# Kernel optimization log

Measured on AMD Instinct MI355X. Metric: run time of the kernel, lower is better.

The kernel has to match this reference:

```python
import jax, jax.numpy as jnp
import numpy as np

B, S, D_MODEL = 2, 2048, 1024
NUM_HEADS = 16
D_HEAD = D_MODEL // NUM_HEADS
THETA = 10000.0


def setup_inputs() -> dict:
    key = jax.random.key(0)
    ks = jax.random.split(key, 5)
    std = float(np.sqrt(2.0 / (D_MODEL + D_MODEL)))
    return {
        "x": jax.random.normal(ks[0], (B, S, D_MODEL), dtype=jnp.float32),
        "wq": jax.random.normal(ks[1], (D_MODEL, D_MODEL), dtype=jnp.float32) * std,
        "wk": jax.random.normal(ks[2], (D_MODEL, D_MODEL), dtype=jnp.float32) * std,
        "wv": jax.random.normal(ks[3], (D_MODEL, D_MODEL), dtype=jnp.float32) * std,
        "wo": jax.random.normal(ks[4], (D_MODEL, D_MODEL), dtype=jnp.float32) * std,
    }


def _apply_rope(x):
    # x: [b, h, s, d]; interleaved even/odd RoPE rotation
    d = x.shape[-1]
    s = x.shape[-2]
    inv_freq = 1.0 / (THETA ** (jnp.arange(0, d, 2, dtype=x.dtype) / d))  # [d/2]
    pos = jnp.arange(s, dtype=x.dtype)
    freqs = pos[:, None] * inv_freq[None, :]  # [s, d/2]
    cos, sin = jnp.cos(freqs), jnp.sin(freqs)
    x_even = x[..., 0::2]
    x_odd = x[..., 1::2]
    rot_even = x_even * cos - x_odd * sin
    rot_odd = x_even * sin + x_odd * cos
    # interleave back: stack pairs on a new trailing axis then flatten
    return jnp.stack([rot_even, rot_odd], axis=-1).reshape(x.shape)


def reference(x, wq, wk, wv, wo):
    b, s, _ = x.shape
    # Linear applies weight [d_out, d_in] as x @ W^T
    q = jnp.einsum('bsd,ed->bse', x, wq)
    k = jnp.einsum('bsd,ed->bse', x, wk)
    v = jnp.einsum('bsd,ed->bse', x, wv)
    # [b, s, h*dh] -> [b, h, s, dh]
    q = q.reshape(b, s, NUM_HEADS, D_HEAD).transpose(0, 2, 1, 3)
    k = k.reshape(b, s, NUM_HEADS, D_HEAD).transpose(0, 2, 1, 3)
    v = v.reshape(b, s, NUM_HEADS, D_HEAD).transpose(0, 2, 1, 3)
    q = _apply_rope(q)
    k = _apply_rope(k)
    scores = jnp.einsum('bhqd,bhkd->bhqk', q, k) / jnp.sqrt(jnp.asarray(D_HEAD, x.dtype))
    causal = jnp.tril(jnp.ones((s, s), dtype=bool))  # allowed positions
    scores = jnp.where(causal, scores, -jnp.inf)
    attn = jax.nn.softmax(scores, axis=-1)
    out = jnp.einsum('bhqk,bhkd->bhqd', attn, v)
    out = out.transpose(0, 2, 1, 3).reshape(b, s, NUM_HEADS * D_HEAD)
    return jnp.einsum('bsd,ed->bse', out, wo)
```

## Files before the change

### kernel.cpp

```cpp
#include <hip/hip_runtime.h>
#include <stdint.h>

typedef unsigned short u16;
typedef __attribute__((ext_vector_type(8))) short bf16x8;
typedef __attribute__((ext_vector_type(4))) short bf16x4;
typedef __attribute__((ext_vector_type(4))) float f32x4;
typedef __attribute__((ext_vector_type(4))) unsigned short u16x4;
typedef __attribute__((ext_vector_type(2))) unsigned u32x2;

#define S_ 2048
#define E_ 1024
#define QSCALE 0.18033688011112042f

__device__ __forceinline__ u16 f2bf(float f) {
  union { float f; unsigned u; } v; v.f = f;
  unsigned u = v.u;
  unsigned r = (u + 0x7FFFu + ((u >> 16) & 1u)) >> 16;
  return (u16)r;
}
__device__ __forceinline__ float bf2f(u16 h) {
  union { unsigned u; float f; } v; v.u = ((unsigned)h) << 16;
  return v.f;
}
__device__ __forceinline__ unsigned cvtpk(float a, float b) {
  unsigned r;
  asm("v_cvt_pk_bf16_f32 %0, %1, %2" : "=v"(r) : "v"(a), "v"(b));
  return r;
}
__device__ __forceinline__ bf16x4 pk4(float a, float b, float c, float d) {
  union { u32x2 u; bf16x4 v; } U;
  U.u[0] = cvtpk(a, b);
  U.u[1] = cvtpk(c, d);
  return U.v;
}

typedef __attribute__((address_space(3))) void lds_void;
__device__ __forceinline__ unsigned lds_off(void* p) {
  return (unsigned)(unsigned long long)(lds_void*)p;
}
__device__ __forceinline__ void glds16(const u16* g, u16* l) {
  __builtin_amdgcn_global_load_lds(
      (const __attribute__((address_space(1))) void*)g,
      (__attribute__((address_space(3))) void*)l, 16, 0, 0);
}

__global__ void k_cast5(const float* __restrict__ x,
                        const float* __restrict__ wq, const float* __restrict__ wk,
                        const float* __restrict__ wv, const float* __restrict__ wo,
                        u16* __restrict__ xb, u16* __restrict__ wqb, u16* __restrict__ wkb,
                        u16* __restrict__ wvb, u16* __restrict__ wob) {
  int i = blockIdx.x * blockDim.x + threadIdx.x;
  const float* src; u16* dst; int off;
  if (i < 1048576) { src = x; dst = xb; off = i; }
  else {
    int j = i - 1048576;
    int w = j >> 18; off = j & 262143;
    src = (w == 0) ? wq : (w == 1) ? wk : (w == 2) ? wv : wo;
    dst = (w == 0) ? wqb : (w == 1) ? wkb : (w == 2) ? wvb : wob;
  }
  float4 v = *((const float4*)src + off);
  u16x4 o;
  o.x = f2bf(v.x); o.y = f2bf(v.y); o.z = f2bf(v.z); o.w = f2bf(v.w);
  *((u16x4*)dst + off) = o;
}

__global__ __launch_bounds__(256) void k_gemm(
    const u16* __restrict__ A,
    const u16* __restrict__ W0, const u16* __restrict__ W1, const u16* __restrict__ W2,
    void* O0, void* O1, void* O2, int outF32)
{
  __shared__ __align__(16) u16 As[2][128 * 32];
  __shared__ __align__(16) u16 Ws[2][128 * 32];
  int tid = threadIdx.x;
  int wid = tid >> 6, lane = tid & 63;
  int lg = lane >> 4, lr = lane & 15;
  int wsel = blockIdx.y >> 3, nb = blockIdx.y & 7;
  const u16* W = (wsel == 0) ? W0 : ((wsel == 1) ? W1 : W2);
  void* O = (wsel == 0) ? O0 : ((wsel == 1) ? O1 : O2);
  int m0 = blockIdx.x * 128;
  int n0 = nb * 128;
  int wr = wid >> 1, wc = wid & 1;

  f32x4 acc[4][4];
#pragma unroll
  for (int m = 0; m < 4; m++)
#pragma unroll
    for (int n = 0; n < 4; n++) acc[m][n] = (f32x4){0.f, 0.f, 0.f, 0.f};

  int srow = tid >> 2;
  int schunk = (tid & 3) ^ ((tid >> 3) & 3);
  const u16* ag = A + (size_t)(m0 + srow) * 1024 + schunk * 8;
  const u16* wg = W + (size_t)(n0 + srow) * 1024 + schunk * 8;

  int buf = 0;
  glds16(ag, &As[0][tid * 8]);
  glds16(ag + 65536, &As[0][tid * 8 + 2048]);
  glds16(wg, &Ws[0][tid * 8]);
  glds16(wg + 65536, &Ws[0][tid * 8 + 2048]);
  __syncthreads();

  for (int kt = 0; kt < 1024; kt += 32) {
    if (kt + 32 < 1024) {
      glds16(ag + kt + 32, &As[buf ^ 1][tid * 8]);
      glds16(ag + kt + 32 + 65536, &As[buf ^ 1][tid * 8 + 2048]);
      glds16(wg + kt + 32, &Ws[buf ^ 1][tid * 8]);
      glds16(wg + kt + 32 + 65536, &Ws[buf ^ 1][tid * 8 + 2048]);
    }
    bf16x8 af[4], wf[4];
#pragma unroll
    for (int m = 0; m < 4; m++) {
      int row = wr * 64 + m * 16 + lr;
      af[m] = *(const bf16x8*)&As[buf][row * 32 + ((lg ^ ((row >> 1) & 3)) * 8)];
    }
#pragma unroll
    for (int n = 0; n < 4; n++) {
      int row = wc * 64 + n * 16 + lr;
      wf[n] = *(const bf16x8*)&Ws[buf][row * 32 + ((lg ^ ((row >> 1) & 3)) * 8)];
    }
    __builtin_amdgcn_s_setprio(1);
#pragma unroll
    for (int m = 0; m < 4; m++)
#pragma unroll
      for (int n = 0; n < 4; n++)
        acc[m][n] = __builtin_amdgcn_mfma_f32_16x16x32_bf16(af[m], wf[n], acc[m][n], 0, 0, 0);
    __builtin_amdgcn_s_setprio(0);
    __syncthreads();
    buf ^= 1;
  }

#pragma unroll
  for (int m = 0; m < 4; m++) {
    int gr = m0 + wr * 64 + m * 16 + lg * 4;
#pragma unroll
    for (int n = 0; n < 4; n++) {
      int gc = n0 + wc * 64 + n * 16 + lr;
#pragma unroll
      for (int r = 0; r < 4; r++) {
        if (outF32) ((float*)O)[(size_t)(gr + r) * 1024 + gc] = acc[m][n][r];
        else ((u16*)O)[(size_t)(gr + r) * 1024 + gc] = f2bf(acc[m][n][r]);
      }
    }
  }
}

__global__ void k_rope(u16* __restrict__ Q, u16* __restrict__ K) {
  int idx = blockIdx.x * blockDim.x + threadIdx.x;
  int p = idx & 511;
  int srow = idx >> 9;
  int s = srow & (S_ - 1);
  int i = p & 31;
  float ang = (float)s * exp2f(-0.415241012f * (float)i);
  float sn, c;
  __sincosf(ang, &sn, &c);
  unsigned* qp = (unsigned*)Q + idx;
  unsigned qv = *qp;
  float e = bf2f((u16)(qv & 0xffff)), o = bf2f((u16)(qv >> 16));
  float re = (e * c - o * sn) * QSCALE, ro = (e * sn + o * c) * QSCALE;
  *qp = cvtpk(re, ro);
  unsigned* kp = (unsigned*)K + idx;
  unsigned kv = *kp;
  e = bf2f((u16)(kv & 0xffff)); o = bf2f((u16)(kv >> 16));
  re = e * c - o * sn; ro = e * sn + o * c;
  *kp = cvtpk(re, ro);
}

__global__ __launch_bounds__(256) void k_attn(
    const u16* __restrict__ Q, const u16* __restrict__ K,
    const u16* __restrict__ V, u16* __restrict__ AO)
{
  __shared__ __align__(16) u16 Ks[64 * 64];
  __shared__ __align__(16) u16 Vs[64 * 64];
  int tid = threadIdx.x;
  int wid = tid >> 6, lane = tid & 63;
  int lg = lane >> 4, lr = lane & 15;
  int bh = blockIdx.x;
  int qb = 15 - (int)blockIdx.y;
  int q0 = qb * 128 + wid * 32;
  size_t base = (size_t)(bh >> 4) * (2048u * 1024u) + (size_t)(bh & 15) * 64;

  const u16* qrow = Q + base + (size_t)(q0 + lr) * 1024 + lg * 8;
  bf16x8 qf0a = *(const bf16x8*)(qrow);
  bf16x8 qf1a = *(const bf16x8*)(qrow + 32);
  bf16x8 qf0b = *(const bf16x8*)(qrow + 16 * 1024);
  bf16x8 qf1b = *(const bf16x8*)(qrow + 16 * 1024 + 32);

  int srow = tid >> 3;
  int sch = tid & 7;
  const u16* kg = K + base + (size_t)srow * 1024 + sch * 8;
  const u16* vg = V + base + (size_t)srow * 1024 + sch * 8;
  int kwb0 = ((srow)*128 + sch * 16) ^ ((srow & 7) << 4);
  int kwb1 = ((srow + 32) * 128 + sch * 16) ^ ((srow & 7) << 4);
  int vwi0 = (srow >> 4) * 1024 + (sch >> 1) * 256 + (srow & 15) * 16 + (sch & 1) * 8;
  int vwi1 = ((srow + 32) >> 4) * 1024 + (sch >> 1) * 256 + (srow & 15) * 16 + (sch & 1) * 8;

  bf16x8 kr0 = *(const bf16x8*)(kg);
  bf16x8 kr1 = *(const bf16x8*)(kg + 32 * 1024);
  bf16x8 vr0 = *(const bf16x8*)(vg);
  bf16x8 vr1 = *(const bf16x8*)(vg + 32 * 1024);
  const u16* kgp = kg + 64 * 1024;
  const u16* vgp = vg + 64 * 1024;

  float ma = -1e30f, mb = -1e30f, lsa = 0.f, lsb = 0.f;
  f32x4 oa[4], ob[4];
#pragma unroll
  for (int c = 0; c < 4; c++) {
    oa[c] = (f32x4){0.f, 0.f, 0.f, 0.f};
    ob[c] = (f32x4){0.f, 0.f, 0.f, 0.f};
  }

  int qga = q0 + lr;
  int qgb = q0 + 16 + lr;
  int ntw = (q0 >> 6) + 1;
  int ntb = 2 * qb + 2;
  unsigned vrd = lds_off(Vs) + (unsigned)(lane * 8);

  for (int t = 0; t < ntb; ++t) {
    __syncthreads();
    *(bf16x8*)((char*)Ks + kwb0) = kr0;
    *(bf16x8*)((char*)Ks + kwb1) = kr1;
    *(bf16x8*)(&Vs[vwi0]) = vr0;
    *(bf16x8*)(&Vs[vwi1]) = vr1;
    __syncthreads();
    if (t + 1 < ntb) {
      kr0 = *(const bf16x8*)(kgp);
      kr1 = *(const bf16x8*)(kgp + 32 * 1024);
      vr0 = *(const bf16x8*)(vgp);
      vr1 = *(const bf16x8*)(vgp + 32 * 1024);
      kgp += 64 * 1024;
      vgp += 64 * 1024;
    }
    if (t >= ntw) continue;

    f32x4 sa[4], sb[4];
    int kv0 = t * 64;
    __builtin_amdgcn_s_setprio(1);
#pragma unroll
    for (int sub = 0; sub < 4; ++sub) {
      int row = sub * 16 + lr;
      int swz = (row & 7) << 4;
      bf16x8 kf0 = *(const bf16x8*)((const char*)Ks + ((row * 128 + lg * 16) ^ swz));
      bf16x8 kf1 = *(const bf16x8*)((const char*)Ks + ((row * 128 + 64 + lg * 16) ^ swz));
      f32x4 z = (f32x4){0.f, 0.f, 0.f, 0.f};
      z = __builtin_amdgcn_mfma_f32_16x16x32_bf16(kf0, qf0a, z, 0, 0, 0);
      sa[sub] = __builtin_amdgcn_mfma_f32_16x16x32_bf16(kf1, qf1a, z, 0, 0, 0);
      f32x4 z2 = (f32x4){0.f, 0.f, 0.f, 0.f};
      z2 = __builtin_amdgcn_mfma_f32_16x16x32_bf16(kf0, qf0b, z2, 0, 0, 0);
      sb[sub] = __builtin_amdgcn_mfma_f32_16x16x32_bf16(kf1, qf1b, z2, 0, 0, 0);
    }
    __builtin_amdgcn_s_setprio(0);
    if (t == ntw - 1) {
#pragma unroll
      for (int sub = 0; sub < 4; ++sub)
#pragma unroll
        for (int j = 0; j < 4; ++j) {
          int kvg = kv0 + sub * 16 + lg * 4 + j;
          sa[sub][j] = (kvg <= qga) ? sa[sub][j] : -1e30f;
          sb[sub][j] = (kvg <= qgb) ? sb[sub][j] : -1e30f;
        }
    }
    float tma = fmaxf(fmaxf(fmaxf(sa[0][0], sa[0][1]), fmaxf(sa[0][2], sa[0][3])),
                      fmaxf(fmaxf(sa[1][0], sa[1][1]), fmaxf(sa[1][2], sa[1][3])));
    tma = fmaxf(tma, fmaxf(fmaxf(fmaxf(sa[2][0], sa[2][1]), fmaxf(sa[2][2], sa[2][3])),
                           fmaxf(fmaxf(sa[3][0], sa[3][1]), fmaxf(sa[3][2], sa[3][3]))));
    float tmb = fmaxf(fmaxf(fmaxf(sb[0][0], sb[0][1]), fmaxf(sb[0][2], sb[0][3])),
                      fmaxf(fmaxf(sb[1][0], sb[1][1]), fmaxf(sb[1][2], sb[1][3])));
    tmb = fmaxf(tmb, fmaxf(fmaxf(fmaxf(sb[2][0], sb[2][1]), fmaxf(sb[2][2], sb[2][3])),
                           fmaxf(fmaxf(sb[3][0], sb[3][1]), fmaxf(sb[3][2], sb[3][3]))));
    tma = fmaxf(tma, __shfl_xor(tma, 16));
    tma = fmaxf(tma, __shfl_xor(tma, 32));
    tmb = fmaxf(tmb, __shfl_xor(tmb, 16));
    tmb = fmaxf(tmb, __shfl_xor(tmb, 32));
    if (!__all((tma <= ma + 8.f) && (tmb <= mb + 8.f))) {
      float mna = fmaxf(ma, tma), mnb = fmaxf(mb, tmb);
      float ca = __builtin_amdgcn_exp2f(ma - mna);
      float cb = __builtin_amdgcn_exp2f(mb - mnb);
      ma = mna; mb = mnb;
      lsa *= ca; lsb *= cb;
#pragma unroll
      for (int c = 0; c < 4; ++c) {
        oa[c][0] *= ca; oa[c][1] *= ca; oa[c][2] *= ca; oa[c][3] *= ca;
        ob[c][0] *= cb; ob[c][1] *= cb; ob[c][2] *= cb; ob[c][3] *= cb;
      }
    }
    bf16x4 pa[4], pb[4];
#pragma unroll
    for (int sub = 0; sub < 4; ++sub) {
      float a0 = __builtin_amdgcn_exp2f(sa[sub][0] - ma);
      float a1 = __builtin_amdgcn_exp2f(sa[sub][1] - ma);
      float a2 = __builtin_amdgcn_exp2f(sa[sub][2] - ma);
      float a3 = __builtin_amdgcn_exp2f(sa[sub][3] - ma);
      lsa += (a0 + a1) + (a2 + a3);
      pa[sub] = pk4(a0, a1, a2, a3);
      float b0 = __builtin_amdgcn_exp2f(sb[sub][0] - mb);
      float b1 = __builtin_amdgcn_exp2f(sb[sub][1] - mb);
      float b2 = __builtin_amdgcn_exp2f(sb[sub][2] - mb);
      float b3 = __builtin_amdgcn_exp2f(sb[sub][3] - mb);
      lsb += (b0 + b1) + (b2 + b3);
      pb[sub] = pk4(b0, b1, b2, b3);
    }
#pragma unroll
    for (int sub = 0; sub < 4; ++sub) {
      unsigned wa = vrd + (unsigned)(sub * 2048);
      bf16x4 va0, va1, va2, va3;
      asm volatile("ds_read_b64_tr_b16 %0, %1" : "=v"(va0) : "v"(wa));
      asm volatile("ds_read_b64_tr_b16 %0, %1 offset:512" : "=v"(va1) : "v"(wa));
      asm volatile("ds_read_b64_tr_b16 %0, %1 offset:1024" : "=v"(va2) : "v"(wa));
      asm volatile("ds_read_b64_tr_b16 %0, %1 offset:1536" : "=v"(va3) : "v"(wa));
      asm volatile("s_waitcnt lgkmcnt(0)" ::: "memory");
      __builtin_amdgcn_sched_barrier(0);
      __builtin_amdgcn_s_setprio(1);
      oa[0] = __builtin_amdgcn_mfma_f32_16x16x16bf16_1k(va0, pa[sub], oa[0], 0, 0, 0);
      oa[1] = __builtin_amdgcn_mfma_f32_16x16x16bf16_1k(va1, pa[sub], oa[1], 0, 0, 0);
      oa[2] = __builtin_amdgcn_mfma_f32_16x16x16bf16_1k(va2, pa[sub], oa[2], 0, 0, 0);
      oa[3] = __builtin_amdgcn_mfma_f32_16x16x16bf16_1k(va3, pa[sub], oa[3], 0, 0, 0);
      ob[0] = __builtin_amdgcn_mfma_f32_16x16x16bf16_1k(va0, pb[sub], ob[0], 0, 0, 0);
      ob[1] = __builtin_amdgcn_mfma_f32_16x16x16bf16_1k(va1, pb[sub], ob[1], 0, 0, 0);
      ob[2] = __builtin_amdgcn_mfma_f32_16x16x16bf16_1k(va2, pb[sub], ob[2], 0, 0, 0);
      ob[3] = __builtin_amdgcn_mfma_f32_16x16x16bf16_1k(va3, pb[sub], ob[3], 0, 0, 0);
      __builtin_amdgcn_s_setprio(0);
    }
  }

  float lta = lsa + __shfl_xor(lsa, 16);
  lta += __shfl_xor(lta, 32);
  float ltb = lsb + __shfl_xor(lsb, 16);
  ltb += __shfl_xor(ltb, 32);
  float inva = 1.0f / lta;
  float invb = 1.0f / ltb;
  u16* orowa = AO + base + (size_t)(q0 + lr) * 1024;
  u16* orowb = orowa + 16 * 1024;
#pragma unroll
  for (int c = 0; c < 4; c++) {
    u32x2 pka, pkb;
    pka[0] = cvtpk(oa[c][0] * inva, oa[c][1] * inva);
    pka[1] = cvtpk(oa[c][2] * inva, oa[c][3] * inva);
    *(u32x2*)&orowa[c * 16 + lg * 4] = pka;
    pkb[0] = cvtpk(ob[c][0] * invb, ob[c][1] * invb);
    pkb[1] = cvtpk(ob[c][2] * invb, ob[c][3] * invb);
    *(u32x2*)&orowb[c * 16 + lg * 4] = pkb;
  }
}

extern "C" void kernel_launch(void* const* d_in, const int* in_sizes, int n_in,
                              void* d_out, int out_size, void* d_ws, size_t ws_size,
                              hipStream_t stream) {
  const float* x = (const float*)d_in[0];
  const float* wq = (const float*)d_in[1];
  const float* wk = (const float*)d_in[2];
  const float* wv = (const float*)d_in[3];
  const float* wo = (const float*)d_in[4];

  char* ws = (char*)d_ws;
  u16* xb  = (u16*)(ws);
  u16* wqb = (u16*)(ws + 8388608);
  u16* wkb = (u16*)(ws + 10485760);
  u16* wvb = (u16*)(ws + 12582912);
  u16* wob = (u16*)(ws + 14680064);
  u16* Qb  = (u16*)(ws + 16777216);
  u16* Kb  = (u16*)(ws + 25165824);
  u16* Vb  = (u16*)(ws + 33554432);
  u16* AO  = (u16*)(ws + 41943040);

  k_cast5<<<8192, 256, 0, stream>>>(x, wq, wk, wv, wo, xb, wqb, wkb, wvb, wob);
  k_gemm<<<dim3(32, 24), 256, 0, stream>>>(xb, wqb, wkb, wvb, Qb, Kb, Vb, 0);
  k_rope<<<8192, 256, 0, stream>>>(Qb, Kb);
  k_attn<<<dim3(32, 16), 256, 0, stream>>>(Qb, Kb, Vb, AO);
  k_gemm<<<dim3(32, 8), 256, 0, stream>>>(AO, wob, wob, wob, d_out, d_out, d_out, 1);
}
```

Baseline: 127.5 us.

## Split causal attention KV range into two partitions and merge partials

```diff
diff --git a/kernel.cpp b/kernel.cpp
--- a/kernel.cpp
+++ b/kernel.cpp
@@ -7,6 +7,7 @@
 typedef __attribute__((ext_vector_type(4))) float f32x4;
 typedef __attribute__((ext_vector_type(4))) unsigned short u16x4;
 typedef __attribute__((ext_vector_type(2))) unsigned u32x2;
+typedef __attribute__((ext_vector_type(4))) unsigned u32x4;
 
 #define S_ 2048
 #define E_ 1024
@@ -166,7 +167,8 @@
 
 __global__ __launch_bounds__(256) void k_attn(
     const u16* __restrict__ Q, const u16* __restrict__ K,
-    const u16* __restrict__ V, u16* __restrict__ AO)
+    const u16* __restrict__ V, u16* __restrict__ AO,
+    u16* __restrict__ P0o, float* __restrict__ P0ml, float* __restrict__ P1ml)
 {
   __shared__ __align__(16) u16 Ks[64 * 64];
   __shared__ __align__(16) u16 Vs[64 * 64];
@@ -174,9 +176,20 @@
   int wid = tid >> 6, lane = tid & 63;
   int lg = lane >> 4, lr = lane & 15;
   int bh = blockIdx.x;
-  int qb = 15 - (int)blockIdx.y;
+  int by = blockIdx.y;
+  int qb = 15 - (by >> 1);
+  int part = by & 1;
+  int ntb = 2 * qb + 2;
+  int h = qb + 1;
+  int t0 = part ? h : 0;
+  int t1 = part ? ntb : h;
   int q0 = qb * 128 + wid * 32;
+  int ntw = 2 * qb + (wid >> 1) + 1;
   size_t base = (size_t)(bh >> 4) * (2048u * 1024u) + (size_t)(bh & 15) * 64;
+  int mlbase = ((bh >> 4) * 2048) * 16 + (bh & 15);
+
+  u16* Oraw = part ? AO : P0o;
+  float* Pml = part ? P1ml : P0ml;
 
   const u16* qrow = Q + base + (size_t)(q0 + lr) * 1024 + lg * 8;
   bf16x8 qf0a = *(const bf16x8*)(qrow);
@@ -186,8 +199,8 @@
 
   int srow = tid >> 3;
   int sch = tid & 7;
-  const u16* kg = K + base + (size_t)srow * 1024 + sch * 8;
-  const u16* vg = V + base + (size_t)srow * 1024 + sch * 8;
+  const u16* kg = K + base + (size_t)srow * 1024 + sch * 8 + (size_t)t0 * 65536;
+  const u16* vg = V + base + (size_t)srow * 1024 + sch * 8 + (size_t)t0 * 65536;
   int kwb0 = ((srow)*128 + sch * 16) ^ ((srow & 7) << 4);
   int kwb1 = ((srow + 32) * 128 + sch * 16) ^ ((srow & 7) << 4);
   int vwi0 = (srow >> 4) * 1024 + (sch >> 1) * 256 + (srow & 15) * 16 + (sch & 1) * 8;
@@ -203,25 +216,23 @@
   float ma = -1e30f, mb = -1e30f, lsa = 0.f, lsb = 0.f;
   f32x4 oa[4], ob[4];
 #pragma unroll
-  for (int c = 0; c < 4; c++) {
-    oa[c] = (f32x4){0.f, 0.f, 0.f, 0.f};
-    ob[c] = (f32x4){0.f, 0.f, 0.f, 0.f};
+  for (int cc = 0; cc < 4; cc++) {
+    oa[cc] = (f32x4){0.f, 0.f, 0.f, 0.f};
+    ob[cc] = (f32x4){0.f, 0.f, 0.f, 0.f};
   }
 
   int qga = q0 + lr;
   int qgb = q0 + 16 + lr;
-  int ntw = (q0 >> 6) + 1;
-  int ntb = 2 * qb + 2;
   unsigned vrd = lds_off(Vs) + (unsigned)(lane * 8);
 
-  for (int t = 0; t < ntb; ++t) {
+  for (int t = t0; t < t1; ++t) {
     __syncthreads();
     *(bf16x8*)((char*)Ks + kwb0) = kr0;
     *(bf16x8*)((char*)Ks + kwb1) = kr1;
     *(bf16x8*)(&Vs[vwi0]) = vr0;
     *(bf16x8*)(&Vs[vwi1]) = vr1;
     __syncthreads();
-    if (t + 1 < ntb) {
+    if (t + 1 < t1) {
       kr0 = *(const bf16x8*)(kgp);
       kr1 = *(const bf16x8*)(kgp + 32 * 1024);
       vr0 = *(const bf16x8*)(vgp);
@@ -277,9 +288,9 @@
       ma = mna; mb = mnb;
       lsa *= ca; lsb *= cb;
 #pragma unroll
-      for (int c = 0; c < 4; ++c) {
-        oa[c][0] *= ca; oa[c][1] *= ca; oa[c][2] *= ca; oa[c][3] *= ca;
-        ob[c][0] *= cb; ob[c][1] *= cb; ob[c][2] *= cb; ob[c][3] *= cb;
+      for (int cc = 0; cc < 4; ++cc) {
+        oa[cc][0] *= ca; oa[cc][1] *= ca; oa[cc][2] *= ca; oa[cc][3] *= ca;
+        ob[cc][0] *= cb; ob[cc][1] *= cb; ob[cc][2] *= cb; ob[cc][3] *= cb;
       }
     }
     bf16x4 pa[4], pb[4];
@@ -325,20 +336,51 @@
   lta += __shfl_xor(lta, 32);
   float ltb = lsb + __shfl_xor(lsb, 16);
   ltb += __shfl_xor(ltb, 32);
-  float inva = 1.0f / lta;
-  float invb = 1.0f / ltb;
-  u16* orowa = AO + base + (size_t)(q0 + lr) * 1024;
+  u16* orowa = Oraw + base + (size_t)(q0 + lr) * 1024;
   u16* orowb = orowa + 16 * 1024;
 #pragma unroll
-  for (int c = 0; c < 4; c++) {
+  for (int cc = 0; cc < 4; cc++) {
     u32x2 pka, pkb;
-    pka[0] = cvtpk(oa[c][0] * inva, oa[c][1] * inva);
-    pka[1] = cvtpk(oa[c][2] * inva, oa[c][3] * inva);
-    *(u32x2*)&orowa[c * 16 + lg * 4] = pka;
-    pkb[0] = cvtpk(ob[c][0] * invb, ob[c][1] * invb);
-    pkb[1] = cvtpk(ob[c][2] * invb, ob[c][3] * invb);
-    *(u32x2*)&orowb[c * 16 + lg * 4] = pkb;
-  }
+    pka[0] = cvtpk(oa[cc][0], oa[cc][1]);
+    pka[1] = cvtpk(oa[cc][2], oa[cc][3]);
+    *(u32x2*)&orowa[cc * 16 + lg * 4] = pka;
+    pkb[0] = cvtpk(ob[cc][0], ob[cc][1]);
+    pkb[1] = cvtpk(ob[cc][2], ob[cc][3]);
+    *(u32x2*)&orowb[cc * 16 + lg * 4] = pkb;
+  }
+  if (lg == 0) {
+    int r2a = (mlbase + (q0 + lr) * 16) * 2;
+    int r2b = (mlbase + (q0 + 16 + lr) * 16) * 2;
+    Pml[r2a] = ma;
+    Pml[r2a + 1] = lta;
+    Pml[r2b] = mb;
+    Pml[r2b + 1] = ltb;
+  }
+}
+
+__global__ void k_merge(u16* __restrict__ AO, const u16* __restrict__ P0o,
+                        const float* __restrict__ P0ml, const float* __restrict__ P1ml) {
+  int idx = blockIdx.x * blockDim.x + threadIdx.x;
+  int r = idx >> 3;
+  int d0 = (idx & 7) * 8;
+  float m0 = P0ml[r * 2], l0 = P0ml[r * 2 + 1];
+  float m1 = P1ml[r * 2], l1 = P1ml[r * 2 + 1];
+  float M = fmaxf(m0, m1);
+  float a0 = __builtin_amdgcn_exp2f(m0 - M);
+  float a1 = __builtin_amdgcn_exp2f(m1 - M);
+  float inv = 1.0f / (l0 * a0 + l1 * a1);
+  float s0 = a0 * inv, s1 = a1 * inv;
+  size_t off = (size_t)(r >> 4) * 1024 + (size_t)(r & 15) * 64 + d0;
+  bf16x8 v0 = *(const bf16x8*)(P0o + off);
+  bf16x8 v1 = *(const bf16x8*)(AO + off);
+  u32x4 outw;
+#pragma unroll
+  for (int j = 0; j < 4; ++j) {
+    float f0 = bf2f((u16)v0[2 * j]) * s0 + bf2f((u16)v1[2 * j]) * s1;
+    float f1 = bf2f((u16)v0[2 * j + 1]) * s0 + bf2f((u16)v1[2 * j + 1]) * s1;
+    outw[j] = cvtpk(f0, f1);
+  }
+  *(u32x4*)(AO + off) = outw;
 }
 
 extern "C" void kernel_launch(void* const* d_in, const int* in_sizes, int n_in,
@@ -360,10 +402,14 @@
   u16* Kb  = (u16*)(ws + 25165824);
   u16* Vb  = (u16*)(ws + 33554432);
   u16* AO  = (u16*)(ws + 41943040);
+  u16*   P0o  = (u16*)(ws);
+  float* P0ml = (float*)(ws + 8388608);
+  float* P1ml = (float*)(ws + 9437184);
 
   k_cast5<<<8192, 256, 0, stream>>>(x, wq, wk, wv, wo, xb, wqb, wkb, wvb, wob);
   k_gemm<<<dim3(32, 24), 256, 0, stream>>>(xb, wqb, wkb, wvb, Qb, Kb, Vb, 0);
   k_rope<<<8192, 256, 0, stream>>>(Qb, Kb);
-  k_attn<<<dim3(32, 16), 256, 0, stream>>>(Qb, Kb, Vb, AO);
+  k_attn<<<dim3(32, 32), 256, 0, stream>>>(Qb, Kb, Vb, AO, P0o, P0ml, P1ml);
+  k_merge<<<2048, 256, 0, stream>>>(AO, P0o, P0ml, P1ml);
   k_gemm<<<dim3(32, 8), 256, 0, stream>>>(AO, wob, wob, wob, d_out, d_out, d_out, 1);
 }
```

Result: faster. 123.1 us (-3.5%).
